# Optimization experiments

Measured on AMD Instinct MI355X. Metric: run time of the kernel, lower is better.

## Reference

```python
import jax, jax.numpy as jnp
import numpy as np

B, S = 128, 32
C = [4, 8, 16, 32]
DN = ('NDHWC', 'DHWIO', 'NDHWC')


def _conv(x, w, stride=1, pad=None):
    k = w.shape[0]
    if pad is None:
        pad = [((k - 1) // 2, k // 2)] * 3  # k=3 -> (1,1); k=4 -> (1,2) as in scn even-kernel convention
    return jax.lax.conv_general_dilated(x, w, (stride,) * 3, pad, dimension_numbers=DN)


def _bn_relu(x, g, b, mask, eps=1e-4):
    # BatchNormLeakyReLU with leakiness=0 (ReLU); stats over ACTIVE voxels only, per channel
    cnt = jnp.maximum(mask.sum(), 1.0)
    mean = (x * mask).sum(axis=(0, 1, 2, 3)) / cnt
    var = (((x - mean) ** 2) * mask).sum(axis=(0, 1, 2, 3)) / cnt
    y = (x - mean) * jax.lax.rsqrt(var + eps) * g + b
    return jnp.maximum(y, 0.0) * mask


def _pool_mask(m):
    # scn.Convolution k=2 s=2: output site active iff any input in its 2^3 receptive field is active
    return jax.lax.reduce_window(m, 0.0, jax.lax.max, (1, 2, 2, 2, 1), (1, 2, 2, 2, 1), 'VALID')


def _up_mask(m):
    # scn.FullConvolution k=2 s=2: each active input activates its full 2^3 output block
    return jnp.repeat(jnp.repeat(jnp.repeat(m, 2, 1), 2, 2), 2, 3)


def _encoder(vox, maskraw, wp, enc, dec, wo):
    mask = (maskraw == 0).astype(vox.dtype)
    x = vox * mask
    x = _conv(x, wp) * mask  # prepare: submanifold conv 1 -> m=4
    for (g, b, ws, wd) in enc:  # 3 non-empty encoding stages (i < num_strides-1)
        x = _bn_relu(x, g, b, mask)
        x = _conv(x, ws) * mask               # submanifold conv k=3
        x = _conv(x, wd, stride=2, pad=[(0, 0)] * 3)  # strided Convolution k=2 s=2
        mask = _pool_mask(mask)
        x = x * mask
    # SparseToDense + view(-1, C*s^3) in NCDHW layout
    hidden = jnp.transpose(x, (0, 4, 1, 2, 3)).reshape(x.shape[0], -1)
    for (g, b, wu, ws3, ws4) in dec:  # i = 2, 1, 0
        x = _bn_relu(x, g, b, mask)
        x = jax.lax.conv_transpose(x, wu, (2, 2, 2), 'VALID', dimension_numbers=DN)  # FullConvolution
        mask = _up_mask(mask)
        x = x * mask
        x = _conv(x, ws3) * mask              # submanifold conv k=3 (end of decoding_conv1)
        mask = mask * (x[..., :1] > 0).astype(x.dtype)  # SparsifyFCS (applied twice; idempotent)
        x = x * mask
        x = _conv(x, ws4) * mask              # submanifold conv k=4 (decoding_conv2)
    out = _conv(x, wo) * mask                 # output: submanifold conv m -> 1
    return hidden, out


def setup_inputs():
    key = jax.random.key(0)
    ks = iter(jax.random.split(key, 64))

    def rnd(shape, s=0.1):
        return jax.random.normal(next(ks), shape, jnp.float32) * s

    inp = {}
    inp['vox'] = jax.random.normal(next(ks), (B, S, S, S, 1), jnp.float32)
    inp['maskraw'] = jax.random.randint(next(ks), (B, S, S, S, 1), 0, 10, jnp.int32)
    inp['wp'] = rnd((3, 3, 3, 1, C[0]))
    for i in range(3):
        ci, co = C[i], C[i + 1]
        inp[f'g_e{i}'] = 1.0 + rnd((ci,))
        inp[f'b_e{i}'] = rnd((ci,))
        inp[f'ws_e{i}'] = rnd((3, 3, 3, ci, ci))
        inp[f'wd_e{i}'] = rnd((2, 2, 2, ci, co))
    for j, i in enumerate([2, 1, 0]):
        ci, co = C[i + 1], C[i]
        inp[f'g_d{j}'] = 1.0 + rnd((ci,))
        inp[f'b_d{j}'] = rnd((ci,))
        inp[f'wu_d{j}'] = rnd((2, 2, 2, ci, co))
        inp[f'ws3_d{j}'] = rnd((3, 3, 3, co, co))
        inp[f'ws4_d{j}'] = rnd((4, 4, 4, co, co))
    inp['wo'] = rnd((3, 3, 3, C[0], 1))
    return inp


def reference(vox, maskraw, wp, g_e0, b_e0, ws_e0, wd_e0, g_e1, b_e1, ws_e1, wd_e1, g_e2, b_e2, ws_e2, wd_e2, g_d0, b_d0, wu_d0, ws3_d0, ws4_d0, g_d1, b_d1, wu_d1, ws3_d1, ws4_d1, g_d2, b_d2, wu_d2, ws3_d2, ws4_d2, wo):
    enc = [(g_e0, b_e0, ws_e0, wd_e0), (g_e1, b_e1, ws_e1, wd_e1), (g_e2, b_e2, ws_e2, wd_e2)]
    dec = [(g_d0, b_d0, wu_d0, ws3_d0, ws4_d0), (g_d1, b_d1, wu_d1, ws3_d1, ws4_d1), (g_d2, b_d2, wu_d2, ws3_d2, ws4_d2)]
    return _encoder(vox, maskraw, wp, enc, dec, wo)
```

## Files before the change

### kernel.cpp

```cpp
#include <hip/hip_runtime.h>

using u8 = unsigned char;

__global__ void mask_init_k(const int* __restrict__ mr, u8* __restrict__ m, int N) {
    int i = blockIdx.x * blockDim.x + threadIdx.x;
    if (i < N) m[i] = (mr[i] == 0) ? 1 : 0;
}

template <int SO>
__global__ void pool_k(const u8* __restrict__ mi, u8* __restrict__ mo) {
    const int N = 128 * SO * SO * SO;
    constexpr int SI = 2 * SO;
    int v = blockIdx.x * blockDim.x + threadIdx.x;
    if (v >= N) return;
    int t = v;
    int x = t % SO; t /= SO;
    int y = t % SO; t /= SO;
    int z = t % SO;
    int n = t / SO;
    u8 m = 0;
    for (int kd = 0; kd < 2; kd++)
        for (int kh = 0; kh < 2; kh++)
            for (int kw = 0; kw < 2; kw++)
                m |= mi[((n * SI + 2 * z + kd) * SI + 2 * y + kh) * SI + 2 * x + kw];
    mo[v] = m;
}


__global__ void prep4t_k(const float* __restrict__ vox, const u8* __restrict__ m,
                         const float* __restrict__ wp, float* __restrict__ out) {
    __shared__ float til[6 * 10 * 35];
    int bid = blockIdx.x;
    int y0 = (bid & 3) << 3, z0 = ((bid >> 2) & 7) << 2, n = bid >> 5;
    for (int t = threadIdx.x; t < 6 * 10 * 35; t += 256) {
        int x_ = t % 35;
        int rr = t / 35;
        int yy = rr % 10, zz = rr / 10;
        int gx = x_ - 1, gy = y0 + yy - 1, gz = z0 + zz - 1;
        float v = 0.f;
        if ((unsigned)gx < 32u && (unsigned)gy < 32u && (unsigned)gz < 32u) {
            int gi = ((n * 32 + gz) * 32 + gy) * 32 + gx;
            if (m[gi]) v = vox[gi];
        }
        til[t] = v;
    }
    __syncthreads();
    int tx = threadIdx.x;
    int xg = tx & 7, ly = (tx >> 3) & 7, lz = tx >> 6;
    int xb = xg << 2;
    int vbase = ((n * 32 + z0 + lz) * 32 + y0 + ly) * 32 + xb;
    u8 om[4];
#pragma unroll
    for (int j = 0; j < 4; j++) om[j] = m[vbase + j];
    float acc[4][4];
#pragma unroll
    for (int j = 0; j < 4; j++)
#pragma unroll
        for (int co = 0; co < 4; co++) acc[j][co] = 0.f;
    for (int kd = 0; kd < 3; kd++) {
        for (int kh = 0; kh < 3; kh++) {
            const float* rowp = &til[((lz + kd) * 10 + ly + kh) * 35 + xb];
            float col[6];
#pragma unroll
            for (int c = 0; c < 6; c++) col[c] = rowp[c];
            const float* wrow = wp + ((kd * 3 + kh) * 3) * 4;
#pragma unroll
            for (int kw = 0; kw < 3; kw++) {
                const float* wt = wrow + kw * 4;
#pragma unroll
                for (int j = 0; j < 4; j++) {
                    float xv = col[j + kw];
#pragma unroll
                    for (int co = 0; co < 4; co++) acc[j][co] += xv * wt[co];
                }
            }
        }
    }
#pragma unroll
    for (int j = 0; j < 4; j++)
#pragma unroll
        for (int co = 0; co < 4; co++)
            out[(size_t)(vbase + j) * 4 + co] = om[j] ? acc[j][co] : 0.f;
}

__global__ void convbn4t_k(const float* __restrict__ in, const float* __restrict__ w,
                           const u8* __restrict__ mask, const double* __restrict__ params,
                           float* __restrict__ out) {
    __shared__ float4 til[6 * 10 * 35];
    float sc[4], sh[4];
#pragma unroll
    for (int c = 0; c < 4; c++) { sc[c] = (float)params[c]; sh[c] = (float)params[4 + c]; }
    int bid = blockIdx.x;
    int y0 = (bid & 3) << 3, z0 = ((bid >> 2) & 7) << 2, n = bid >> 5;
    for (int t = threadIdx.x; t < 6 * 10 * 35; t += 256) {
        int x_ = t % 35;
        int rr = t / 35;
        int yy = rr % 10, zz = rr / 10;
        int gx = x_ - 1, gy = y0 + yy - 1, gz = z0 + zz - 1;
        float4 v = make_float4(0.f, 0.f, 0.f, 0.f);
        if ((unsigned)gx < 32u && (unsigned)gy < 32u && (unsigned)gz < 32u) {
            int gi = ((n * 32 + gz) * 32 + gy) * 32 + gx;
            if (mask[gi]) {
                float4 r = *(const float4*)(in + (size_t)gi * 4);
                v.x = fmaxf(r.x * sc[0] + sh[0], 0.f);
                v.y = fmaxf(r.y * sc[1] + sh[1], 0.f);
                v.z = fmaxf(r.z * sc[2] + sh[2], 0.f);
                v.w = fmaxf(r.w * sc[3] + sh[3], 0.f);
            }
        }
        til[t] = v;
    }
    __syncthreads();
    int tx = threadIdx.x;
    int xg = tx & 7, ly = (tx >> 3) & 7, lz = tx >> 6;
    int xb = xg << 2;
    int vbase = ((n * 32 + z0 + lz) * 32 + y0 + ly) * 32 + xb;
    u8 om[4];
#pragma unroll
    for (int j = 0; j < 4; j++) om[j] = mask[vbase + j];
    float acc[4][4];
#pragma unroll
    for (int j = 0; j < 4; j++)
#pragma unroll
        for (int co = 0; co < 4; co++) acc[j][co] = 0.f;
    for (int kd = 0; kd < 3; kd++) {
        for (int kh = 0; kh < 3; kh++) {
            const float4* rowp = &til[((lz + kd) * 10 + ly + kh) * 35 + xb];
            float col[6][4];
#pragma unroll
            for (int c = 0; c < 6; c++) {
                float4 t4 = rowp[c];
                col[c][0] = t4.x; col[c][1] = t4.y; col[c][2] = t4.z; col[c][3] = t4.w;
            }
            const float* wrow = w + ((kd * 3 + kh) * 3) * 16;
#pragma unroll
            for (int kw = 0; kw < 3; kw++) {
                const float* wt = wrow + kw * 16;
#pragma unroll
                for (int j = 0; j < 4; j++) {
#pragma unroll
                    for (int ci = 0; ci < 4; ci++) {
                        float xv = col[j + kw][ci];
#pragma unroll
                        for (int co = 0; co < 4; co++) acc[j][co] += xv * wt[ci * 4 + co];
                    }
                }
            }
        }
    }
#pragma unroll
    for (int j = 0; j < 4; j++)
#pragma unroll
        for (int co = 0; co < 4; co++)
            out[(size_t)(vbase + j) * 4 + co] = om[j] ? acc[j][co] : 0.f;
}

__global__ void conv3s4t_k(const float* __restrict__ in, const float* __restrict__ w,
                           const u8* __restrict__ pmask, u8* __restrict__ nmask,
                           float* __restrict__ out, double delta) {
    __shared__ float4 til[6 * 10 * 35];
    int bid = blockIdx.x;
    int y0 = (bid & 3) << 3, z0 = ((bid >> 2) & 7) << 2, n = bid >> 5;
    for (int t = threadIdx.x; t < 6 * 10 * 35; t += 256) {
        int x_ = t % 35;
        int rr = t / 35;
        int yy = rr % 10, zz = rr / 10;
        int gx = x_ - 1, gy = y0 + yy - 1, gz = z0 + zz - 1;
        float4 v = make_float4(0.f, 0.f, 0.f, 0.f);
        if ((unsigned)gx < 32u && (unsigned)gy < 32u && (unsigned)gz < 32u)
            v = *(const float4*)(in + (size_t)(((n * 32 + gz) * 32 + gy) * 32 + gx) * 4);
        til[t] = v;
    }
    __syncthreads();
    int tx = threadIdx.x;
    int xg = tx & 7, ly = (tx >> 3) & 7, lz = tx >> 6;
    int xb = xg << 2;
    int gy = y0 + ly, gz = z0 + lz;
    int vbase = ((n * 32 + gz) * 32 + gy) * 32 + xb;
    int pbase = ((n * 16 + (gz >> 1)) * 16 + (gy >> 1)) * 16 + (xb >> 1);
    u8 pm[4];
    pm[0] = pm[1] = pmask[pbase];
    pm[2] = pm[3] = pmask[pbase + 1];
    double acc0[4], asum[4];
    float accf[4][4];
#pragma unroll
    for (int j = 0; j < 4; j++) {
        acc0[j] = 0.0; asum[j] = 0.0;
#pragma unroll
        for (int co = 0; co < 4; co++) accf[j][co] = 0.f;
    }
    for (int kd = 0; kd < 3; kd++) {
        for (int kh = 0; kh < 3; kh++) {
            const float4* rowp = &til[((lz + kd) * 10 + ly + kh) * 35 + xb];
            float col[6][4];
#pragma unroll
            for (int c = 0; c < 6; c++) {
                float4 t4 = rowp[c];
                col[c][0] = t4.x; col[c][1] = t4.y; col[c][2] = t4.z; col[c][3] = t4.w;
            }
            const float* wrow = w + ((kd * 3 + kh) * 3) * 16;
#pragma unroll
            for (int kw = 0; kw < 3; kw++) {
                const float* wt = wrow + kw * 16;
#pragma unroll
                for (int j = 0; j < 4; j++) {
#pragma unroll
                    for (int ci = 0; ci < 4; ci++) {
                        float xv = col[j + kw][ci];
                        double term = (double)xv * (double)wt[ci * 4 + 0];
                        acc0[j] += term;
                        asum[j] += fabs(term);
#pragma unroll
                        for (int co = 1; co < 4; co++) accf[j][co] += xv * wt[ci * 4 + co];
                    }
                }
            }
        }
    }
#pragma unroll
    for (int j = 0; j < 4; j++) {
        u8 nm = (pm[j] && (acc0[j] > -delta * asum[j])) ? 1 : 0;
        nmask[vbase + j] = nm;
        out[(size_t)(vbase + j) * 4 + 0] = nm ? (float)acc0[j] : 0.f;
#pragma unroll
        for (int co = 1; co < 4; co++) out[(size_t)(vbase + j) * 4 + co] = nm ? accf[j][co] : 0.f;
    }
}

__global__ void conv4x4t_k(const float* __restrict__ in, const float* __restrict__ w,
                           const u8* __restrict__ outmask, float* __restrict__ out) {
    __shared__ float4 til[7 * 11 * 35];
    int bid = blockIdx.x;
    int y0 = (bid & 3) << 3, z0 = ((bid >> 2) & 7) << 2, n = bid >> 5;
    for (int t = threadIdx.x; t < 7 * 11 * 35; t += 256) {
        int x_ = t % 35;
        int rr = t / 35;
        int yy = rr % 11, zz = rr / 11;
        int gx = x_ - 1, gy = y0 + yy - 1, gz = z0 + zz - 1;
        float4 v = make_float4(0.f, 0.f, 0.f, 0.f);
        if ((unsigned)gx < 32u && (unsigned)gy < 32u && (unsigned)gz < 32u)
            v = *(const float4*)(in + (size_t)(((n * 32 + gz) * 32 + gy) * 32 + gx) * 4);
        til[t] = v;
    }
    __syncthreads();
    int tx = threadIdx.x;
    int xg = tx & 7, ly = (tx >> 3) & 7, lz = tx >> 6;
    int xb = xg << 2;
    int vbase = ((n * 32 + z0 + lz) * 32 + y0 + ly) * 32 + xb;
    u8 om[4];
#pragma unroll
    for (int j = 0; j < 4; j++) om[j] = outmask[vbase + j];
    float acc[4][4];
#pragma unroll
    for (int j = 0; j < 4; j++)
#pragma unroll
        for (int co = 0; co < 4; co++) acc[j][co] = 0.f;
    for (int kd = 0; kd < 4; kd++) {
        for (int kh = 0; kh < 4; kh++) {
            const float4* rowp = &til[((lz + kd) * 11 + ly + kh) * 35 + xb];
            float col[7][4];
#pragma unroll
            for (int c = 0; c < 7; c++) {
                float4 t4 = rowp[c];
                col[c][0] = t4.x; col[c][1] = t4.y; col[c][2] = t4.z; col[c][3] = t4.w;
            }
            const float* wrow = w + ((kd * 4 + kh) * 4) * 16;
#pragma unroll
            for (int kw = 0; kw < 4; kw++) {
                const float* wt = wrow + kw * 16;
#pragma unroll
                for (int j = 0; j < 4; j++) {
#pragma unroll
                    for (int ci = 0; ci < 4; ci++) {
                        float xv = col[j + kw][ci];
#pragma unroll
                        for (int co = 0; co < 4; co++) acc[j][co] += xv * wt[ci * 4 + co];
                    }
                }
            }
        }
    }
#pragma unroll
    for (int j = 0; j < 4; j++)
#pragma unroll
        for (int co = 0; co < 4; co++)
            out[(size_t)(vbase + j) * 4 + co] = om[j] ? acc[j][co] : 0.f;
}

__global__ void outconv4t_k(const float* __restrict__ in, const float* __restrict__ w,
                            const u8* __restrict__ mask, float* __restrict__ out) {
    __shared__ float4 til[6 * 10 * 35];
    int bid = blockIdx.x;
    int y0 = (bid & 3) << 3, z0 = ((bid >> 2) & 7) << 2, n = bid >> 5;
    for (int t = threadIdx.x; t < 6 * 10 * 35; t += 256) {
        int x_ = t % 35;
        int rr = t / 35;
        int yy = rr % 10, zz = rr / 10;
        int gx = x_ - 1, gy = y0 + yy - 1, gz = z0 + zz - 1;
        float4 v = make_float4(0.f, 0.f, 0.f, 0.f);
        if ((unsigned)gx < 32u && (unsigned)gy < 32u && (unsigned)gz < 32u)
            v = *(const float4*)(in + (size_t)(((n * 32 + gz) * 32 + gy) * 32 + gx) * 4);
        til[t] = v;
    }
    __syncthreads();
    int tx = threadIdx.x;
    int xg = tx & 7, ly = (tx >> 3) & 7, lz = tx >> 6;
    int xb = xg << 2;
    int vbase = ((n * 32 + z0 + lz) * 32 + y0 + ly) * 32 + xb;
    u8 om[4];
#pragma unroll
    for (int j = 0; j < 4; j++) om[j] = mask[vbase + j];
    float acc[4] = {0.f, 0.f, 0.f, 0.f};
    for (int kd = 0; kd < 3; kd++) {
        for (int kh = 0; kh < 3; kh++) {
            const float4* rowp = &til[((lz + kd) * 10 + ly + kh) * 35 + xb];
            float col[6][4];
#pragma unroll
            for (int c = 0; c < 6; c++) {
                float4 t4 = rowp[c];
                col[c][0] = t4.x; col[c][1] = t4.y; col[c][2] = t4.z; col[c][3] = t4.w;
            }
            const float* wrow = w + ((kd * 3 + kh) * 3) * 4;
#pragma unroll
            for (int kw = 0; kw < 3; kw++) {
                const float* wt = wrow + kw * 4;
#pragma unroll
                for (int j = 0; j < 4; j++) {
#pragma unroll
                    for (int ci = 0; ci < 4; ci++) acc[j] += col[j + kw][ci] * wt[ci];
                }
            }
        }
    }
#pragma unroll
    for (int j = 0; j < 4; j++) out[vbase + j] = om[j] ? acc[j] : 0.f;
}


__global__ void convbn8_k(const float* __restrict__ in, const float* __restrict__ w,
                          const u8* __restrict__ mask, const double* __restrict__ params,
                          float* __restrict__ out) {
    __shared__ float4 til[4][330];
    __shared__ float wl[27 * 256];
    float sc[16], sh[16];
#pragma unroll
    for (int c = 0; c < 16; c++) { sc[c] = (float)params[c]; sh[c] = (float)params[16 + c]; }
    int z = blockIdx.x & 7, n = blockIdx.x >> 3;
    for (int t = threadIdx.x; t < 27 * 256; t += 256) wl[t] = w[t];
    for (int t = threadIdx.x; t < 300; t += 256) {
        int xx = t % 10;
        int rr = t / 10;
        int yy = rr % 10, zz = rr / 10;
        int gx = xx - 1, gy = yy - 1, gz = z + zz - 1;
        float v[16];
#pragma unroll
        for (int c = 0; c < 16; c++) v[c] = 0.f;
        if ((unsigned)gx < 8u && (unsigned)gy < 8u && (unsigned)gz < 8u) {
            int gi = ((n * 8 + gz) * 8 + gy) * 8 + gx;
            if (mask[gi]) {
                const float* ip = in + (size_t)gi * 16;
#pragma unroll
                for (int c = 0; c < 16; c++) v[c] = fmaxf(ip[c] * sc[c] + sh[c], 0.f);
            }
        }
        int s = (zz * 10 + yy) * 11 + xx;
#pragma unroll
        for (int q = 0; q < 4; q++)
            til[q][s] = make_float4(v[4 * q], v[4 * q + 1], v[4 * q + 2], v[4 * q + 3]);
    }
    __syncthreads();
    int x = threadIdx.x & 7, y = (threadIdx.x >> 3) & 7, cq = threadIdx.x >> 6;
    int v = ((n * 8 + z) * 8 + y) * 8 + x;
    u8 om = mask[v];
    float acc[4] = {0.f, 0.f, 0.f, 0.f};
    for (int kd = 0; kd < 3; kd++) {
        for (int kh = 0; kh < 3; kh++) {
            int rbase = (kd * 10 + y + kh) * 11 + x;
            const float* wrow = wl + ((kd * 3 + kh) * 3) * 256;
#pragma unroll
            for (int kw = 0; kw < 3; kw++) {
                int s = rbase + kw;
                float4 q0 = til[0][s], q1 = til[1][s], q2 = til[2][s], q3 = til[3][s];
                float xs[16] = {q0.x, q0.y, q0.z, q0.w, q1.x, q1.y, q1.z, q1.w,
                                q2.x, q2.y, q2.z, q2.w, q3.x, q3.y, q3.z, q3.w};
                const float* wt = wrow + kw * 256 + cq * 4;
#pragma unroll
                for (int ci = 0; ci < 16; ci++) {
                    float xv = xs[ci];
                    float4 w4 = *(const float4*)(wt + ci * 16);
                    acc[0] += xv * w4.x; acc[1] += xv * w4.y;
                    acc[2] += xv * w4.z; acc[3] += xv * w4.w;
                }
            }
        }
    }
    float* op = out + (size_t)v * 16 + cq * 4;
#pragma unroll
    for (int j = 0; j < 4; j++) op[j] = om ? acc[j] : 0.f;
}

__global__ void conv3s8_k(const float* __restrict__ in, const float* __restrict__ w,
                          const u8* __restrict__ pmask, u8* __restrict__ nmask,
                          float* __restrict__ out, double delta) {
    __shared__ float4 til[4][330];
    __shared__ float wl[27 * 256];
    __shared__ u8 nmsh[64];
    int z = blockIdx.x & 7, n = blockIdx.x >> 3;
    for (int t = threadIdx.x; t < 27 * 256; t += 256) wl[t] = w[t];
    for (int t = threadIdx.x; t < 300; t += 256) {
        int xx = t % 10;
        int rr = t / 10;
        int yy = rr % 10, zz = rr / 10;
        int gx = xx - 1, gy = yy - 1, gz = z + zz - 1;
        float4 v0 = make_float4(0.f, 0.f, 0.f, 0.f), v1 = v0, v2 = v0, v3 = v0;
        if ((unsigned)gx < 8u && (unsigned)gy < 8u && (unsigned)gz < 8u) {
            const float4* ip = (const float4*)(in + (size_t)(((n * 8 + gz) * 8 + gy) * 8 + gx) * 16);
            v0 = ip[0]; v1 = ip[1]; v2 = ip[2]; v3 = ip[3];
        }
        int s = (zz * 10 + yy) * 11 + xx;
        til[0][s] = v0; til[1][s] = v1; til[2][s] = v2; til[3][s] = v3;
    }
    __syncthreads();
    int x = threadIdx.x & 7, y = (threadIdx.x >> 3) & 7, cq = threadIdx.x >> 6;
    int v = ((n * 8 + z) * 8 + y) * 8 + x;
    double acc0 = 0.0, asum = 0.0;
    float acc[4] = {0.f, 0.f, 0.f, 0.f};
    for (int kd = 0; kd < 3; kd++) {
        for (int kh = 0; kh < 3; kh++) {
            int rbase = (kd * 10 + y + kh) * 11 + x;
            const float* wrow = wl + ((kd * 3 + kh) * 3) * 256;
#pragma unroll
            for (int kw = 0; kw < 3; kw++) {
                int s = rbase + kw;
                float4 q0 = til[0][s], q1 = til[1][s], q2 = til[2][s], q3 = til[3][s];
                float xs[16] = {q0.x, q0.y, q0.z, q0.w, q1.x, q1.y, q1.z, q1.w,
                                q2.x, q2.y, q2.z, q2.w, q3.x, q3.y, q3.z, q3.w};
                const float* wt0 = wrow + kw * 256;
                if (cq == 0) {
#pragma unroll
                    for (int ci = 0; ci < 16; ci++) {
                        float xv = xs[ci];
                        double term = (double)xv * (double)wt0[ci * 16];
                        acc0 += term;
                        asum += fabs(term);
#pragma unroll
                        for (int j = 1; j < 4; j++) acc[j] += xv * wt0[ci * 16 + j];
                    }
                } else {
                    const float* wt = wt0 + cq * 4;
#pragma unroll
                    for (int ci = 0; ci < 16; ci++) {
                        float xv = xs[ci];
                        float4 w4 = *(const float4*)(wt + ci * 16);
                        acc[0] += xv * w4.x; acc[1] += xv * w4.y;
                        acc[2] += xv * w4.z; acc[3] += xv * w4.w;
                    }
                }
            }
        }
    }
    if (cq == 0) {
        u8 pm = pmask[((n * 4 + (z >> 1)) * 4 + (y >> 1)) * 4 + (x >> 1)];
        u8 nm = (pm && (acc0 > -delta * asum)) ? 1 : 0;
        nmsh[y * 8 + x] = nm;
        nmask[v] = nm;
    }
    __syncthreads();
    u8 nm = nmsh[y * 8 + x];
    float* op = out + (size_t)v * 16 + cq * 4;
    if (cq == 0) {
        op[0] = nm ? (float)acc0 : 0.f;
#pragma unroll
        for (int j = 1; j < 4; j++) op[j] = nm ? acc[j] : 0.f;
    } else {
#pragma unroll
        for (int j = 0; j < 4; j++) op[j] = nm ? acc[j] : 0.f;
    }
}

__global__ void conv48_k(const float* __restrict__ in, const float* __restrict__ w,
                         const u8* __restrict__ outmask, float* __restrict__ out) {
    __shared__ float4 til[4][572];
    __shared__ float wl[16 * 256];
    int z = blockIdx.x & 7, n = blockIdx.x >> 3;
    for (int t = threadIdx.x; t < 484; t += 256) {
        int xx = t % 11;
        int rr = t / 11;
        int yy = rr % 11, zz = rr / 11;
        int gx = xx - 1, gy = yy - 1, gz = z + zz - 1;
        float4 v0 = make_float4(0.f, 0.f, 0.f, 0.f), v1 = v0, v2 = v0, v3 = v0;
        if ((unsigned)gx < 8u && (unsigned)gy < 8u && (unsigned)gz < 8u) {
            const float4* ip = (const float4*)(in + (size_t)(((n * 8 + gz) * 8 + gy) * 8 + gx) * 16);
            v0 = ip[0]; v1 = ip[1]; v2 = ip[2]; v3 = ip[3];
        }
        int s = (zz * 11 + yy) * 13 + xx;
        til[0][s] = v0; til[1][s] = v1; til[2][s] = v2; til[3][s] = v3;
    }
    int x = threadIdx.x & 7, y = (threadIdx.x >> 3) & 7, cq = threadIdx.x >> 6;
    int v = ((n * 8 + z) * 8 + y) * 8 + x;
    u8 om = outmask[v];
    float acc[4] = {0.f, 0.f, 0.f, 0.f};
    for (int kd = 0; kd < 4; kd++) {
        __syncthreads();
        for (int t = threadIdx.x; t < 16 * 256; t += 256) wl[t] = w[kd * 16 * 256 + t];
        __syncthreads();
        for (int kh = 0; kh < 4; kh++) {
            int rbase = (kd * 11 + y + kh) * 13 + x;
            const float* wrow = wl + (kh * 4) * 256;
#pragma unroll
            for (int kw = 0; kw < 4; kw++) {
                int s = rbase + kw;
                float4 q0 = til[0][s], q1 = til[1][s], q2 = til[2][s], q3 = til[3][s];
                float xs[16] = {q0.x, q0.y, q0.z, q0.w, q1.x, q1.y, q1.z, q1.w,
                                q2.x, q2.y, q2.z, q2.w, q3.x, q3.y, q3.z, q3.w};
                const float* wt = wrow + kw * 256 + cq * 4;
#pragma unroll
                for (int ci = 0; ci < 16; ci++) {
                    float xv = xs[ci];
                    float4 w4 = *(const float4*)(wt + ci * 16);
                    acc[0] += xv * w4.x; acc[1] += xv * w4.y;
                    acc[2] += xv * w4.z; acc[3] += xv * w4.w;
                }
            }
        }
    }
    float* op = out + (size_t)v * 16 + cq * 4;
#pragma unroll
    for (int j = 0; j < 4; j++) op[j] = om ? acc[j] : 0.f;
}


template <int K, int CIN, int COUT, int S>
__global__ void conv_k(const float* __restrict__ in, const float* __restrict__ w,
                       const u8* __restrict__ outmask, float* __restrict__ out) {
    __shared__ float wl[K * K * K * CIN * COUT];
    for (int t = threadIdx.x; t < K * K * K * CIN * COUT; t += 256) wl[t] = w[t];
    __syncthreads();
    const int N = 128 * S * S * S;
    int v = blockIdx.x * blockDim.x + threadIdx.x;
    if (v >= N) return;
    if (!outmask[v]) {
#pragma unroll
        for (int co = 0; co < COUT; co++) out[(size_t)v * COUT + co] = 0.f;
        return;
    }
    int t = v;
    int x = t % S; t /= S;
    int y = t % S; t /= S;
    int z = t % S;
    int n = t / S;
    float acc[COUT];
#pragma unroll
    for (int co = 0; co < COUT; co++) acc[co] = 0.f;
    constexpr int PLO = (K - 1) / 2;
    for (int kd = 0; kd < K; kd++) {
        int zz = z + kd - PLO; if ((unsigned)zz >= (unsigned)S) continue;
        for (int kh = 0; kh < K; kh++) {
            int yy = y + kh - PLO; if ((unsigned)yy >= (unsigned)S) continue;
            for (int kw = 0; kw < K; kw++) {
                int xx = x + kw - PLO; if ((unsigned)xx >= (unsigned)S) continue;
                int sv = ((n * S + zz) * S + yy) * S + xx;
                const float* ip = in + (size_t)sv * CIN;
                const float* wpk = wl + ((kd * K + kh) * K + kw) * CIN * COUT;
#pragma unroll
                for (int ci = 0; ci < CIN; ci++) {
                    float xv = ip[ci];
#pragma unroll
                    for (int co = 0; co < COUT; co++) acc[co] += xv * wpk[ci * COUT + co];
                }
            }
        }
    }
#pragma unroll
    for (int co = 0; co < COUT; co++) out[(size_t)v * COUT + co] = acc[co];
}

template <int CIN, int COUT, int S>
__global__ void convbn_k(const float* __restrict__ in, const float* __restrict__ w,
                         const u8* __restrict__ mask, const double* __restrict__ params,
                         float* __restrict__ out) {
    __shared__ float wl[27 * CIN * COUT];
    for (int t = threadIdx.x; t < 27 * CIN * COUT; t += 256) wl[t] = w[t];
    __syncthreads();
    const int N = 128 * S * S * S;
    int v = blockIdx.x * blockDim.x + threadIdx.x;
    if (v >= N) return;
    if (!mask[v]) {
#pragma unroll
        for (int co = 0; co < COUT; co++) out[(size_t)v * COUT + co] = 0.f;
        return;
    }
    int t = v;
    int x = t % S; t /= S;
    int y = t % S; t /= S;
    int z = t % S;
    int n = t / S;
    float sc[CIN], sh[CIN];
#pragma unroll
    for (int c = 0; c < CIN; c++) { sc[c] = (float)params[c]; sh[c] = (float)params[CIN + c]; }
    float acc[COUT];
#pragma unroll
    for (int co = 0; co < COUT; co++) acc[co] = 0.f;
    for (int kd = 0; kd < 3; kd++) {
        int zz = z + kd - 1; if ((unsigned)zz >= (unsigned)S) continue;
        for (int kh = 0; kh < 3; kh++) {
            int yy = y + kh - 1; if ((unsigned)yy >= (unsigned)S) continue;
            for (int kw = 0; kw < 3; kw++) {
                int xx = x + kw - 1; if ((unsigned)xx >= (unsigned)S) continue;
                int sv = ((n * S + zz) * S + yy) * S + xx;
                if (!mask[sv]) continue;
                const float* ip = in + (size_t)sv * CIN;
                const float* wpk = wl + ((kd * 3 + kh) * 3 + kw) * CIN * COUT;
#pragma unroll
                for (int ci = 0; ci < CIN; ci++) {
                    float yv = fmaxf(ip[ci] * sc[ci] + sh[ci], 0.f);
#pragma unroll
                    for (int co = 0; co < COUT; co++) acc[co] += yv * wpk[ci * COUT + co];
                }
            }
        }
    }
#pragma unroll
    for (int co = 0; co < COUT; co++) out[(size_t)v * COUT + co] = acc[co];
}

template <int CIN, int COUT, int S>
__global__ void conv3s_k(const float* __restrict__ in, const float* __restrict__ w,
                         const u8* __restrict__ pmask, u8* __restrict__ nmask,
                         float* __restrict__ out, double delta) {
    __shared__ float wl[27 * CIN * COUT];
    for (int t = threadIdx.x; t < 27 * CIN * COUT; t += 256) wl[t] = w[t];
    __syncthreads();
    const int N = 128 * S * S * S;
    constexpr int SP = S / 2;
    int v = blockIdx.x * blockDim.x + threadIdx.x;
    if (v >= N) return;
    int t = v;
    int x = t % S; t /= S;
    int y = t % S; t /= S;
    int z = t % S;
    int n = t / S;
    int pidx = ((n * SP + (z >> 1)) * SP + (y >> 1)) * SP + (x >> 1);
    if (!pmask[pidx]) {
        nmask[v] = 0;
#pragma unroll
        for (int co = 0; co < COUT; co++) out[(size_t)v * COUT + co] = 0.f;
        return;
    }
    double acc0 = 0.0, asum = 0.0;
    float acc[COUT];
#pragma unroll
    for (int co = 0; co < COUT; co++) acc[co] = 0.f;
    for (int kd = 0; kd < 3; kd++) {
        int zz = z + kd - 1; if ((unsigned)zz >= (unsigned)S) continue;
        for (int kh = 0; kh < 3; kh++) {
            int yy = y + kh - 1; if ((unsigned)yy >= (unsigned)S) continue;
            for (int kw = 0; kw < 3; kw++) {
                int xx = x + kw - 1; if ((unsigned)xx >= (unsigned)S) continue;
                int sv = ((n * S + zz) * S + yy) * S + xx;
                const float* ip = in + (size_t)sv * CIN;
                const float* wpk = wl + ((kd * 3 + kh) * 3 + kw) * CIN * COUT;
#pragma unroll
                for (int ci = 0; ci < CIN; ci++) {
                    float xv = ip[ci];
                    double term = (double)xv * (double)wpk[ci * COUT + 0];
                    acc0 += term;
                    asum += fabs(term);
#pragma unroll
                    for (int co = 1; co < COUT; co++) acc[co] += xv * wpk[ci * COUT + co];
                }
            }
        }
    }
    u8 nm = (acc0 > -delta * asum) ? 1 : 0;
    nmask[v] = nm;
    out[(size_t)v * COUT + 0] = nm ? (float)acc0 : 0.f;
#pragma unroll
    for (int co = 1; co < COUT; co++) out[(size_t)v * COUT + co] = nm ? acc[co] : 0.f;
}

template <int CIN, int COUT, int SO>
__global__ void down_k(const float* __restrict__ in, const float* __restrict__ w,
                       const u8* __restrict__ outmask, float* __restrict__ out) {
    const int N = 128 * SO * SO * SO;
    constexpr int SI = 2 * SO;
    int v = blockIdx.x * blockDim.x + threadIdx.x;
    if (v >= N) return;
    if (!outmask[v]) {
#pragma unroll
        for (int co = 0; co < COUT; co++) out[(size_t)v * COUT + co] = 0.f;
        return;
    }
    int t = v;
    int x = t % SO; t /= SO;
    int y = t % SO; t /= SO;
    int z = t % SO;
    int n = t / SO;
    float acc[COUT];
#pragma unroll
    for (int co = 0; co < COUT; co++) acc[co] = 0.f;
    for (int kd = 0; kd < 2; kd++)
        for (int kh = 0; kh < 2; kh++)
            for (int kw = 0; kw < 2; kw++) {
                int sv = ((n * SI + 2 * z + kd) * SI + 2 * y + kh) * SI + 2 * x + kw;
                const float* ip = in + (size_t)sv * CIN;
                const float* wpk = w + ((kd * 2 + kh) * 2 + kw) * CIN * COUT;
#pragma unroll
                for (int ci = 0; ci < CIN; ci++) {
                    float xv = ip[ci];
#pragma unroll
                    for (int co = 0; co < COUT; co++) acc[co] += xv * wpk[ci * COUT + co];
                }
            }
#pragma unroll
    for (int co = 0; co < COUT; co++) out[(size_t)v * COUT + co] = acc[co];
}

template <int CIN, int COUT, int SI>
__global__ void upbn_k(const float* __restrict__ in, const float* __restrict__ w,
                       const u8* __restrict__ inmask, const double* __restrict__ params,
                       float* __restrict__ out) {
    constexpr int SO = 2 * SI;
    const int N = 128 * SO * SO * SO;
    int v = blockIdx.x * blockDim.x + threadIdx.x;
    if (v >= N) return;
    int t = v;
    int x = t % SO; t /= SO;
    int y = t % SO; t /= SO;
    int z = t % SO;
    int n = t / SO;
    int sv = ((n * SI + (z >> 1)) * SI + (y >> 1)) * SI + (x >> 1);
    if (!inmask[sv]) {
#pragma unroll
        for (int co = 0; co < COUT; co++) out[(size_t)v * COUT + co] = 0.f;
        return;
    }
    int tap = ((1 - (z & 1)) * 2 + (1 - (y & 1))) * 2 + (1 - (x & 1));
    const float* wpk = w + tap * CIN * COUT;
    const float* ip = in + (size_t)sv * CIN;
    float acc[COUT];
#pragma unroll
    for (int co = 0; co < COUT; co++) acc[co] = 0.f;
#pragma unroll
    for (int ci = 0; ci < CIN; ci++) {
        float yv = fmaxf(ip[ci] * (float)params[ci] + (float)params[CIN + ci], 0.f);
#pragma unroll
        for (int co = 0; co < COUT; co++) acc[co] += yv * wpk[ci * COUT + co];
    }
#pragma unroll
    for (int co = 0; co < COUT; co++) out[(size_t)v * COUT + co] = acc[co];
}

template <int C>
__global__ void bn_reduce_k(const float* __restrict__ x, const u8* __restrict__ m, int N,
                            double* __restrict__ partial) {
    double cnt = 0.0, sx[C], s2[C];
#pragma unroll
    for (int c = 0; c < C; c++) { sx[c] = 0.0; s2[c] = 0.0; }
    int stride = gridDim.x * blockDim.x;
    for (int v = blockIdx.x * blockDim.x + threadIdx.x; v < N; v += stride) {
        if (!m[v]) continue;
        cnt += 1.0;
#pragma unroll
        for (int c = 0; c < C; c++) {
            double xv = (double)x[(size_t)v * C + c];
            sx[c] += xv;
            s2[c] += xv * xv;
        }
    }
#pragma unroll
    for (int off = 32; off > 0; off >>= 1) {
        cnt += __shfl_down(cnt, off, 64);
#pragma unroll
        for (int c = 0; c < C; c++) {
            sx[c] += __shfl_down(sx[c], off, 64);
            s2[c] += __shfl_down(s2[c], off, 64);
        }
    }
    __shared__ double sbuf[4][2 * C + 1];
    int wave = threadIdx.x >> 6;
    if ((threadIdx.x & 63) == 0) {
        sbuf[wave][0] = cnt;
#pragma unroll
        for (int c = 0; c < C; c++) {
            sbuf[wave][1 + c] = sx[c];
            sbuf[wave][1 + C + c] = s2[c];
        }
    }
    __syncthreads();
    if (threadIdx.x == 0) {
        double* p = partial + (size_t)blockIdx.x * (2 * C + 1);
        double tcnt = 0.0;
        for (int wv = 0; wv < 4; wv++) tcnt += sbuf[wv][0];
        p[0] = tcnt;
#pragma unroll
        for (int c = 0; c < C; c++) {
            double a = 0.0, b = 0.0;
            for (int wv = 0; wv < 4; wv++) { a += sbuf[wv][1 + c]; b += sbuf[wv][1 + C + c]; }
            p[1 + c] = a;
            p[1 + C + c] = b;
        }
    }
}

template <int C>
__global__ void bn_final_k(const double* __restrict__ partial, int nblocks,
                           const float* __restrict__ g, const float* __restrict__ b,
                           double* __restrict__ params) {
    int c = threadIdx.x;
    if (c >= C) return;
    double cnt = 0.0, sx = 0.0, s2 = 0.0;
    for (int bk = 0; bk < nblocks; bk++) {
        const double* p = partial + (size_t)bk * (2 * C + 1);
        cnt += p[0];
        sx += p[1 + c];
        s2 += p[1 + C + c];
    }
    if (cnt < 1.0) cnt = 1.0;
    double mean = sx / cnt;
    double var = s2 / cnt - mean * mean;
    double sc = (double)g[c] / sqrt(var + 1e-4);
    params[c] = sc;
    params[C + c] = (double)b[c] - mean * sc;
}

__global__ void hidden_k(const float* __restrict__ x, float* __restrict__ out) {
    int i = blockIdx.x * blockDim.x + threadIdx.x;
    if (i >= 128 * 2048) return;
    int b = i >> 11;
    int r = i & 2047;
    int c = r >> 6;
    int s = r & 63;
    int d = s >> 4;
    int h = (s >> 2) & 3;
    int w = s & 3;
    out[i] = x[((((b * 4 + d) * 4 + h) * 4 + w) << 5) + c];
}

extern "C" void kernel_launch(void* const* d_in, const int* in_sizes, int n_in,
                              void* d_out, int out_size, void* d_ws, size_t ws_size,
                              hipStream_t stream) {
    const float* vox = (const float*)d_in[0];
    const int* mraw = (const int*)d_in[1];
    const float* wp = (const float*)d_in[2];
    const float* g_e0 = (const float*)d_in[3];
    const float* b_e0 = (const float*)d_in[4];
    const float* ws_e0 = (const float*)d_in[5];
    const float* wd_e0 = (const float*)d_in[6];
    const float* g_e1 = (const float*)d_in[7];
    const float* b_e1 = (const float*)d_in[8];
    const float* ws_e1 = (const float*)d_in[9];
    const float* wd_e1 = (const float*)d_in[10];
    const float* g_e2 = (const float*)d_in[11];
    const float* b_e2 = (const float*)d_in[12];
    const float* ws_e2 = (const float*)d_in[13];
    const float* wd_e2 = (const float*)d_in[14];
    const float* g_d0 = (const float*)d_in[15];
    const float* b_d0 = (const float*)d_in[16];
    const float* wu_d0 = (const float*)d_in[17];
    const float* ws3_d0 = (const float*)d_in[18];
    const float* ws4_d0 = (const float*)d_in[19];
    const float* g_d1 = (const float*)d_in[20];
    const float* b_d1 = (const float*)d_in[21];
    const float* wu_d1 = (const float*)d_in[22];
    const float* ws3_d1 = (const float*)d_in[23];
    const float* ws4_d1 = (const float*)d_in[24];
    const float* g_d2 = (const float*)d_in[25];
    const float* b_d2 = (const float*)d_in[26];
    const float* wu_d2 = (const float*)d_in[27];
    const float* ws3_d2 = (const float*)d_in[28];
    const float* ws4_d2 = (const float*)d_in[29];
    const float* wo = (const float*)d_in[30];
    float* out = (float*)d_out;

    float* wsf = (float*)d_ws;
    size_t offf = 0;
    auto allocf = [&](size_t n) { float* p = wsf + offf; offf += n; return p; };
    float* R1 = allocf(16777216);
    float* R2 = allocf(16777216);
    float* S1 = allocf(1048576);
    float* S2 = allocf(1048576);
    float* T = allocf(262144);
    double* wsd = (double*)(wsf + offf);
    double* partial = wsd;
    double* params = wsd + 16640;
    u8* wsm = (u8*)(wsd + 16640 + 128);
    size_t offm = 0;
    auto allocm = [&](size_t n) { u8* p = wsm + offm; offm += n; return p; };
    u8* m32 = allocm(4194304);
    u8* m16 = allocm(524288);
    u8* m8 = allocm(65536);
    u8* m4 = allocm(8192);
    u8* mD8 = allocm(65536);
    u8* mD16 = allocm(524288);
    u8* mD32 = allocm(4194304);

    const int N32 = 128 * 32768;
    const int N16 = 128 * 4096;
    const int N8 = 128 * 512;
    const int N4 = 128 * 64;
    auto gs = [](int n) { return dim3((n + 255) / 256); };
    auto rbn = [](int n) { int bl = (n + 255) / 256; return bl > 256 ? 256 : bl; };
    dim3 blk(256);
    dim3 tgrid(4096);
    dim3 grid8(1024);

    mask_init_k<<<gs(N32), blk, 0, stream>>>(mraw, m32, N32);
    pool_k<16><<<gs(N16), blk, 0, stream>>>(m32, m16);
    pool_k<8><<<gs(N8), blk, 0, stream>>>(m16, m8);
    pool_k<4><<<gs(N4), blk, 0, stream>>>(m8, m4);

    prep4t_k<<<tgrid, blk, 0, stream>>>(vox, m32, wp, R1);
    int nb0 = rbn(N32);
    bn_reduce_k<4><<<dim3(nb0), blk, 0, stream>>>(R1, m32, N32, partial);
    bn_final_k<4><<<1, 64, 0, stream>>>(partial, nb0, g_e0, b_e0, params);
    convbn4t_k<<<tgrid, blk, 0, stream>>>(R1, ws_e0, m32, params, R2);
    down_k<4, 8, 16><<<gs(N16), blk, 0, stream>>>(R2, wd_e0, m16, R1);

    int nb1 = rbn(N16);
    bn_reduce_k<8><<<dim3(nb1), blk, 0, stream>>>(R1, m16, N16, partial);
    bn_final_k<8><<<1, 64, 0, stream>>>(partial, nb1, g_e1, b_e1, params);
    convbn_k<8, 8, 16><<<gs(N16), blk, 0, stream>>>(R1, ws_e1, m16, params, R2);
    down_k<8, 16, 8><<<gs(N8), blk, 0, stream>>>(R2, wd_e1, m8, S1);

    int nb2 = rbn(N8);
    bn_reduce_k<16><<<dim3(nb2), blk, 0, stream>>>(S1, m8, N8, partial);
    bn_final_k<16><<<1, 64, 0, stream>>>(partial, nb2, g_e2, b_e2, params);
    convbn8_k<<<grid8, blk, 0, stream>>>(S1, ws_e2, m8, params, S2);
    down_k<16, 32, 4><<<gs(N4), blk, 0, stream>>>(S2, wd_e2, m4, T);

    hidden_k<<<gs(128 * 2048), blk, 0, stream>>>(T, out);

    int nb3 = rbn(N4);
    bn_reduce_k<32><<<dim3(nb3), blk, 0, stream>>>(T, m4, N4, partial);
    bn_final_k<32><<<1, 64, 0, stream>>>(partial, nb3, g_d0, b_d0, params);
    upbn_k<32, 16, 4><<<gs(N8), blk, 0, stream>>>(T, wu_d0, m4, params, S1);
    conv3s8_k<<<grid8, blk, 0, stream>>>(S1, ws3_d0, m4, mD8, S2, 4e-7);
    conv48_k<<<grid8, blk, 0, stream>>>(S2, ws4_d0, mD8, S1);

    int nb4 = rbn(N8);
    bn_reduce_k<16><<<dim3(nb4), blk, 0, stream>>>(S1, mD8, N8, partial);
    bn_final_k<16><<<1, 64, 0, stream>>>(partial, nb4, g_d1, b_d1, params);
    upbn_k<16, 8, 8><<<gs(N16), blk, 0, stream>>>(S1, wu_d1, mD8, params, R1);
    conv3s_k<8, 8, 16><<<gs(N16), blk, 0, stream>>>(R1, ws3_d1, mD8, mD16, R2, 4e-7);
    conv_k<4, 8, 8, 16><<<gs(N16), blk, 0, stream>>>(R2, ws4_d1, mD16, R1);

    int nb5 = rbn(N16);
    bn_reduce_k<8><<<dim3(nb5), blk, 0, stream>>>(R1, mD16, N16, partial);
    bn_final_k<8><<<1, 64, 0, stream>>>(partial, nb5, g_d2, b_d2, params);
    upbn_k<8, 4, 16><<<gs(N32), blk, 0, stream>>>(R1, wu_d2, mD16, params, R2);
    conv3s4t_k<<<tgrid, blk, 0, stream>>>(R2, ws3_d2, mD16, mD32, R1, 0.0);
    conv4x4t_k<<<tgrid, blk, 0, stream>>>(R1, ws4_d2, mD32, R2);
    outconv4t_k<<<tgrid, blk, 0, stream>>>(R2, wo, mD32, out + 262144);
}
```

Before: 1.480 ms.

## Add shared-memory tiled convs for 16^3 stage and drop unused asum in 32^3 sparsify

Three per-voxel 16^3 convolution kernels (encoder conv+BN, decoder sparsify conv, decoder k=4 conv) are replaced with tiled versions. Each block stages an input halo tile and the weights in LDS, and each thread computes two voxels along x. This removes redundant global gathers, mask-driven divergence and per-voxel early exits. Separately, the 32^3 sparsify kernel was always called with delta=0, so it now drops the double-precision abs-sum accumulator and tests acc0>0 directly. The tiled kernels compute every voxel, including inactive ones, so they give up the work skipped at roughly 10% occupancy in exchange for regular, coalesced access.

```diff
diff --git a/kernel.cpp b/kernel.cpp
--- a/kernel.cpp
+++ b/kernel.cpp
@@ -157,7 +157,7 @@
 
 __global__ void conv3s4t_k(const float* __restrict__ in, const float* __restrict__ w,
                            const u8* __restrict__ pmask, u8* __restrict__ nmask,
-                           float* __restrict__ out, double delta) {
+                           float* __restrict__ out) {
     __shared__ float4 til[6 * 10 * 35];
     int bid = blockIdx.x;
     int y0 = (bid & 3) << 3, z0 = ((bid >> 2) & 7) << 2, n = bid >> 5;
@@ -181,11 +181,11 @@
     u8 pm[4];
     pm[0] = pm[1] = pmask[pbase];
     pm[2] = pm[3] = pmask[pbase + 1];
-    double acc0[4], asum[4];
+    double acc0[4];
     float accf[4][4];
 #pragma unroll
     for (int j = 0; j < 4; j++) {
-        acc0[j] = 0.0; asum[j] = 0.0;
+        acc0[j] = 0.0;
 #pragma unroll
         for (int co = 0; co < 4; co++) accf[j][co] = 0.f;
     }
@@ -207,9 +207,7 @@
 #pragma unroll
                     for (int ci = 0; ci < 4; ci++) {
                         float xv = col[j + kw][ci];
-                        double term = (double)xv * (double)wt[ci * 4 + 0];
-                        acc0[j] += term;
-                        asum[j] += fabs(term);
+                        acc0[j] += (double)xv * (double)wt[ci * 4 + 0];
 #pragma unroll
                         for (int co = 1; co < 4; co++) accf[j][co] += xv * wt[ci * 4 + co];
                     }
@@ -219,7 +217,7 @@
     }
 #pragma unroll
     for (int j = 0; j < 4; j++) {
-        u8 nm = (pm[j] && (acc0[j] > -delta * asum[j])) ? 1 : 0;
+        u8 nm = (pm[j] && (acc0[j] > 0.0)) ? 1 : 0;
         nmask[vbase + j] = nm;
         out[(size_t)(vbase + j) * 4 + 0] = nm ? (float)acc0[j] : 0.f;
 #pragma unroll
@@ -334,6 +332,218 @@
     }
 #pragma unroll
     for (int j = 0; j < 4; j++) out[vbase + j] = om[j] ? acc[j] : 0.f;
+}
+
+
+__global__ void convbn16t_k(const float* __restrict__ in, const float* __restrict__ w,
+                            const u8* __restrict__ mask, const double* __restrict__ params,
+                            float* __restrict__ out) {
+    __shared__ float4 til[2][1140];
+    __shared__ float wl[1728];
+    float sc[8], sh[8];
+#pragma unroll
+    for (int c = 0; c < 8; c++) { sc[c] = (float)params[c]; sh[c] = (float)params[8 + c]; }
+    int bid = blockIdx.x;
+    int y0 = (bid & 1) << 3, z0 = ((bid >> 1) & 3) << 2, n = bid >> 3;
+    for (int t = threadIdx.x; t < 1728; t += 256) wl[t] = w[t];
+    for (int t = threadIdx.x; t < 1140; t += 256) {
+        int x_ = t % 19;
+        int rr = t / 19;
+        int yy = rr % 10, zz = rr / 10;
+        int gx = x_ - 1, gy = y0 + yy - 1, gz = z0 + zz - 1;
+        float v[8];
+#pragma unroll
+        for (int c = 0; c < 8; c++) v[c] = 0.f;
+        if ((unsigned)gx < 16u && (unsigned)gy < 16u && (unsigned)gz < 16u) {
+            int gi = ((n * 16 + gz) * 16 + gy) * 16 + gx;
+            if (mask[gi]) {
+                const float* ip = in + (size_t)gi * 8;
+#pragma unroll
+                for (int c = 0; c < 8; c++) v[c] = fmaxf(ip[c] * sc[c] + sh[c], 0.f);
+            }
+        }
+        til[0][t] = make_float4(v[0], v[1], v[2], v[3]);
+        til[1][t] = make_float4(v[4], v[5], v[6], v[7]);
+    }
+    __syncthreads();
+    int xg = threadIdx.x & 7, ly = (threadIdx.x >> 3) & 7, lz = threadIdx.x >> 6;
+    int xb = xg << 1;
+    int vbase = ((n * 16 + z0 + lz) * 16 + y0 + ly) * 16 + xb;
+    u8 om[2] = {mask[vbase], mask[vbase + 1]};
+    float acc[2][8];
+#pragma unroll
+    for (int j = 0; j < 2; j++)
+#pragma unroll
+        for (int co = 0; co < 8; co++) acc[j][co] = 0.f;
+    for (int kd = 0; kd < 3; kd++) {
+        for (int kh = 0; kh < 3; kh++) {
+            int rbase = ((lz + kd) * 10 + ly + kh) * 19 + xb;
+            float col[4][8];
+#pragma unroll
+            for (int c = 0; c < 4; c++) {
+                float4 a = til[0][rbase + c], b = til[1][rbase + c];
+                col[c][0] = a.x; col[c][1] = a.y; col[c][2] = a.z; col[c][3] = a.w;
+                col[c][4] = b.x; col[c][5] = b.y; col[c][6] = b.z; col[c][7] = b.w;
+            }
+            const float* wrow = wl + ((kd * 3 + kh) * 3) * 64;
+#pragma unroll
+            for (int kw = 0; kw < 3; kw++) {
+                const float* wt = wrow + kw * 64;
+#pragma unroll
+                for (int j = 0; j < 2; j++) {
+#pragma unroll
+                    for (int ci = 0; ci < 8; ci++) {
+                        float xv = col[j + kw][ci];
+#pragma unroll
+                        for (int co = 0; co < 8; co++) acc[j][co] += xv * wt[ci * 8 + co];
+                    }
+                }
+            }
+        }
+    }
+#pragma unroll
+    for (int j = 0; j < 2; j++)
+#pragma unroll
+        for (int co = 0; co < 8; co++)
+            out[(size_t)(vbase + j) * 8 + co] = om[j] ? acc[j][co] : 0.f;
+}
+
+__global__ void conv3s16t_k(const float* __restrict__ in, const float* __restrict__ w,
+                            const u8* __restrict__ pmask, u8* __restrict__ nmask,
+                            float* __restrict__ out, double delta) {
+    __shared__ float4 til[2][1140];
+    __shared__ float wl[1728];
+    int bid = blockIdx.x;
+    int y0 = (bid & 1) << 3, z0 = ((bid >> 1) & 3) << 2, n = bid >> 3;
+    for (int t = threadIdx.x; t < 1728; t += 256) wl[t] = w[t];
+    for (int t = threadIdx.x; t < 1140; t += 256) {
+        int x_ = t % 19;
+        int rr = t / 19;
+        int yy = rr % 10, zz = rr / 10;
+        int gx = x_ - 1, gy = y0 + yy - 1, gz = z0 + zz - 1;
+        float4 a = make_float4(0.f, 0.f, 0.f, 0.f), b = a;
+        if ((unsigned)gx < 16u && (unsigned)gy < 16u && (unsigned)gz < 16u) {
+            const float4* ip = (const float4*)(in + (size_t)(((n * 16 + gz) * 16 + gy) * 16 + gx) * 8);
+            a = ip[0]; b = ip[1];
+        }
+        til[0][t] = a;
+        til[1][t] = b;
+    }
+    __syncthreads();
+    int xg = threadIdx.x & 7, ly = (threadIdx.x >> 3) & 7, lz = threadIdx.x >> 6;
+    int xb = xg << 1;
+    int gy = y0 + ly, gz = z0 + lz;
+    int vbase = ((n * 16 + gz) * 16 + gy) * 16 + xb;
+    u8 pm = pmask[((n * 8 + (gz >> 1)) * 8 + (gy >> 1)) * 8 + (xb >> 1)];
+    double acc0[2], asum[2];
+    float accf[2][8];
+#pragma unroll
+    for (int j = 0; j < 2; j++) {
+        acc0[j] = 0.0; asum[j] = 0.0;
+#pragma unroll
+        for (int co = 0; co < 8; co++) accf[j][co] = 0.f;
+    }
+    for (int kd = 0; kd < 3; kd++) {
+        for (int kh = 0; kh < 3; kh++) {
+            int rbase = ((lz + kd) * 10 + ly + kh) * 19 + xb;
+            float col[4][8];
+#pragma unroll
+            for (int c = 0; c < 4; c++) {
+                float4 a = til[0][rbase + c], b = til[1][rbase + c];
+                col[c][0] = a.x; col[c][1] = a.y; col[c][2] = a.z; col[c][3] = a.w;
+                col[c][4] = b.x; col[c][5] = b.y; col[c][6] = b.z; col[c][7] = b.w;
+            }
+            const float* wrow = wl + ((kd * 3 + kh) * 3) * 64;
+#pragma unroll
+            for (int kw = 0; kw < 3; kw++) {
+                const float* wt = wrow + kw * 64;
+#pragma unroll
+                for (int j = 0; j < 2; j++) {
+#pragma unroll
+                    for (int ci = 0; ci < 8; ci++) {
+                        float xv = col[j + kw][ci];
+                        double term = (double)xv * (double)wt[ci * 8 + 0];
+                        acc0[j] += term;
+                        asum[j] += fabs(term);
+#pragma unroll
+                        for (int co = 1; co < 8; co++) accf[j][co] += xv * wt[ci * 8 + co];
+                    }
+                }
+            }
+        }
+    }
+#pragma unroll
+    for (int j = 0; j < 2; j++) {
+        u8 nm = (pm && (acc0[j] > -delta * asum[j])) ? 1 : 0;
+        nmask[vbase + j] = nm;
+        out[(size_t)(vbase + j) * 8 + 0] = nm ? (float)acc0[j] : 0.f;
+#pragma unroll
+        for (int co = 1; co < 8; co++) out[(size_t)(vbase + j) * 8 + co] = nm ? accf[j][co] : 0.f;
+    }
+}
+
+__global__ void conv416t_k(const float* __restrict__ in, const float* __restrict__ w,
+                           const u8* __restrict__ outmask, float* __restrict__ out) {
+    __shared__ float4 til[2][1463];
+    __shared__ float wl[1024];
+    int bid = blockIdx.x;
+    int y0 = (bid & 1) << 3, z0 = ((bid >> 1) & 3) << 2, n = bid >> 3;
+    for (int t = threadIdx.x; t < 1463; t += 256) {
+        int x_ = t % 19;
+        int rr = t / 19;
+        int yy = rr % 11, zz = rr / 11;
+        int gx = x_ - 1, gy = y0 + yy - 1, gz = z0 + zz - 1;
+        float4 a = make_float4(0.f, 0.f, 0.f, 0.f), b = a;
+        if ((unsigned)gx < 16u && (unsigned)gy < 16u && (unsigned)gz < 16u) {
+            const float4* ip = (const float4*)(in + (size_t)(((n * 16 + gz) * 16 + gy) * 16 + gx) * 8);
+            a = ip[0]; b = ip[1];
+        }
+        til[0][t] = a;
+        til[1][t] = b;
+    }
+    int xg = threadIdx.x & 7, ly = (threadIdx.x >> 3) & 7, lz = threadIdx.x >> 6;
+    int xb = xg << 1;
+    int vbase = ((n * 16 + z0 + lz) * 16 + y0 + ly) * 16 + xb;
+    u8 om[2] = {outmask[vbase], outmask[vbase + 1]};
+    float acc[2][8];
+#pragma unroll
+    for (int j = 0; j < 2; j++)
+#pragma unroll
+        for (int co = 0; co < 8; co++) acc[j][co] = 0.f;
+    for (int kd = 0; kd < 4; kd++) {
+        __syncthreads();
+        for (int t = threadIdx.x; t < 1024; t += 256) wl[t] = w[kd * 1024 + t];
+        __syncthreads();
+        for (int kh = 0; kh < 4; kh++) {
+            int rbase = ((lz + kd) * 11 + ly + kh) * 19 + xb;
+            float col[5][8];
+#pragma unroll
+            for (int c = 0; c < 5; c++) {
+                float4 a = til[0][rbase + c], b = til[1][rbase + c];
+                col[c][0] = a.x; col[c][1] = a.y; col[c][2] = a.z; col[c][3] = a.w;
+                col[c][4] = b.x; col[c][5] = b.y; col[c][6] = b.z; col[c][7] = b.w;
+            }
+            const float* wrow = wl + (kh * 4) * 64;
+#pragma unroll
+            for (int kw = 0; kw < 4; kw++) {
+                const float* wt = wrow + kw * 64;
+#pragma unroll
+                for (int j = 0; j < 2; j++) {
+#pragma unroll
+                    for (int ci = 0; ci < 8; ci++) {
+                        float xv = col[j + kw][ci];
+#pragma unroll
+                        for (int co = 0; co < 8; co++) acc[j][co] += xv * wt[ci * 8 + co];
+                    }
+                }
+            }
+        }
+    }
+#pragma unroll
+    for (int j = 0; j < 2; j++)
+#pragma unroll
+        for (int co = 0; co < 8; co++)
+            out[(size_t)(vbase + j) * 8 + co] = om[j] ? acc[j][co] : 0.f;
 }
 
 
@@ -529,155 +739,6 @@
     for (int j = 0; j < 4; j++) op[j] = om ? acc[j] : 0.f;
 }
 
-
-template <int K, int CIN, int COUT, int S>
-__global__ void conv_k(const float* __restrict__ in, const float* __restrict__ w,
-                       const u8* __restrict__ outmask, float* __restrict__ out) {
-    __shared__ float wl[K * K * K * CIN * COUT];
-    for (int t = threadIdx.x; t < K * K * K * CIN * COUT; t += 256) wl[t] = w[t];
-    __syncthreads();
-    const int N = 128 * S * S * S;
-    int v = blockIdx.x * blockDim.x + threadIdx.x;
-    if (v >= N) return;
-    if (!outmask[v]) {
-#pragma unroll
-        for (int co = 0; co < COUT; co++) out[(size_t)v * COUT + co] = 0.f;
-        return;
-    }
-    int t = v;
-    int x = t % S; t /= S;
-    int y = t % S; t /= S;
-    int z = t % S;
-    int n = t / S;
-    float acc[COUT];
-#pragma unroll
-    for (int co = 0; co < COUT; co++) acc[co] = 0.f;
-    constexpr int PLO = (K - 1) / 2;
-    for (int kd = 0; kd < K; kd++) {
-        int zz = z + kd - PLO; if ((unsigned)zz >= (unsigned)S) continue;
-        for (int kh = 0; kh < K; kh++) {
-            int yy = y + kh - PLO; if ((unsigned)yy >= (unsigned)S) continue;
-            for (int kw = 0; kw < K; kw++) {
-                int xx = x + kw - PLO; if ((unsigned)xx >= (unsigned)S) continue;
-                int sv = ((n * S + zz) * S + yy) * S + xx;
-                const float* ip = in + (size_t)sv * CIN;
-                const float* wpk = wl + ((kd * K + kh) * K + kw) * CIN * COUT;
-#pragma unroll
-                for (int ci = 0; ci < CIN; ci++) {
-                    float xv = ip[ci];
-#pragma unroll
-                    for (int co = 0; co < COUT; co++) acc[co] += xv * wpk[ci * COUT + co];
-                }
-            }
-        }
-    }
-#pragma unroll
-    for (int co = 0; co < COUT; co++) out[(size_t)v * COUT + co] = acc[co];
-}
-
-template <int CIN, int COUT, int S>
-__global__ void convbn_k(const float* __restrict__ in, const float* __restrict__ w,
-                         const u8* __restrict__ mask, const double* __restrict__ params,
-                         float* __restrict__ out) {
-    __shared__ float wl[27 * CIN * COUT];
-    for (int t = threadIdx.x; t < 27 * CIN * COUT; t += 256) wl[t] = w[t];
-    __syncthreads();
-    const int N = 128 * S * S * S;
-    int v = blockIdx.x * blockDim.x + threadIdx.x;
-    if (v >= N) return;
-    if (!mask[v]) {
-#pragma unroll
-        for (int co = 0; co < COUT; co++) out[(size_t)v * COUT + co] = 0.f;
-        return;
-    }
-    int t = v;
-    int x = t % S; t /= S;
-    int y = t % S; t /= S;
-    int z = t % S;
-    int n = t / S;
-    float sc[CIN], sh[CIN];
-#pragma unroll
-    for (int c = 0; c < CIN; c++) { sc[c] = (float)params[c]; sh[c] = (float)params[CIN + c]; }
-    float acc[COUT];
-#pragma unroll
-    for (int co = 0; co < COUT; co++) acc[co] = 0.f;
-    for (int kd = 0; kd < 3; kd++) {
-        int zz = z + kd - 1; if ((unsigned)zz >= (unsigned)S) continue;
-        for (int kh = 0; kh < 3; kh++) {
-            int yy = y + kh - 1; if ((unsigned)yy >= (unsigned)S) continue;
-            for (int kw = 0; kw < 3; kw++) {
-                int xx = x + kw - 1; if ((unsigned)xx >= (unsigned)S) continue;
-                int sv = ((n * S + zz) * S + yy) * S + xx;
-                if (!mask[sv]) continue;
-                const float* ip = in + (size_t)sv * CIN;
-                const float* wpk = wl + ((kd * 3 + kh) * 3 + kw) * CIN * COUT;
-#pragma unroll
-                for (int ci = 0; ci < CIN; ci++) {
-                    float yv = fmaxf(ip[ci] * sc[ci] + sh[ci], 0.f);
-#pragma unroll
-                    for (int co = 0; co < COUT; co++) acc[co] += yv * wpk[ci * COUT + co];
-                }
-            }
-        }
-    }
-#pragma unroll
-    for (int co = 0; co < COUT; co++) out[(size_t)v * COUT + co] = acc[co];
-}
-
-template <int CIN, int COUT, int S>
-__global__ void conv3s_k(const float* __restrict__ in, const float* __restrict__ w,
-                         const u8* __restrict__ pmask, u8* __restrict__ nmask,
-                         float* __restrict__ out, double delta) {
-    __shared__ float wl[27 * CIN * COUT];
-    for (int t = threadIdx.x; t < 27 * CIN * COUT; t += 256) wl[t] = w[t];
-    __syncthreads();
-    const int N = 128 * S * S * S;
-    constexpr int SP = S / 2;
-    int v = blockIdx.x * blockDim.x + threadIdx.x;
-    if (v >= N) return;
-    int t = v;
-    int x = t % S; t /= S;
-    int y = t % S; t /= S;
-    int z = t % S;
-    int n = t / S;
-    int pidx = ((n * SP + (z >> 1)) * SP + (y >> 1)) * SP + (x >> 1);
-    if (!pmask[pidx]) {
-        nmask[v] = 0;
-#pragma unroll
-        for (int co = 0; co < COUT; co++) out[(size_t)v * COUT + co] = 0.f;
-        return;
-    }
-    double acc0 = 0.0, asum = 0.0;
-    float acc[COUT];
-#pragma unroll
-    for (int co = 0; co < COUT; co++) acc[co] = 0.f;
-    for (int kd = 0; kd < 3; kd++) {
-        int zz = z + kd - 1; if ((unsigned)zz >= (unsigned)S) continue;
-        for (int kh = 0; kh < 3; kh++) {
-            int yy = y + kh - 1; if ((unsigned)yy >= (unsigned)S) continue;
-            for (int kw = 0; kw < 3; kw++) {
-                int xx = x + kw - 1; if ((unsigned)xx >= (unsigned)S) continue;
-                int sv = ((n * S + zz) * S + yy) * S + xx;
-                const float* ip = in + (size_t)sv * CIN;
-                const float* wpk = wl + ((kd * 3 + kh) * 3 + kw) * CIN * COUT;
-#pragma unroll
-                for (int ci = 0; ci < CIN; ci++) {
-                    float xv = ip[ci];
-                    double term = (double)xv * (double)wpk[ci * COUT + 0];
-                    acc0 += term;
-                    asum += fabs(term);
-#pragma unroll
-                    for (int co = 1; co < COUT; co++) acc[co] += xv * wpk[ci * COUT + co];
-                }
-            }
-        }
-    }
-    u8 nm = (acc0 > -delta * asum) ? 1 : 0;
-    nmask[v] = nm;
-    out[(size_t)v * COUT + 0] = nm ? (float)acc0 : 0.f;
-#pragma unroll
-    for (int co = 1; co < COUT; co++) out[(size_t)v * COUT + co] = nm ? acc[co] : 0.f;
-}
 
 template <int CIN, int COUT, int SO>
 __global__ void down_k(const float* __restrict__ in, const float* __restrict__ w,
@@ -903,6 +964,7 @@
     auto rbn = [](int n) { int bl = (n + 255) / 256; return bl > 256 ? 256 : bl; };
     dim3 blk(256);
     dim3 tgrid(4096);
+    dim3 grid16(1024);
     dim3 grid8(1024);
 
     mask_init_k<<<gs(N32), blk, 0, stream>>>(mraw, m32, N32);
@@ -920,7 +982,7 @@
     int nb1 = rbn(N16);
     bn_reduce_k<8><<<dim3(nb1), blk, 0, stream>>>(R1, m16, N16, partial);
     bn_final_k<8><<<1, 64, 0, stream>>>(partial, nb1, g_e1, b_e1, params);
-    convbn_k<8, 8, 16><<<gs(N16), blk, 0, stream>>>(R1, ws_e1, m16, params, R2);
+    convbn16t_k<<<grid16, blk, 0, stream>>>(R1, ws_e1, m16, params, R2);
     down_k<8, 16, 8><<<gs(N8), blk, 0, stream>>>(R2, wd_e1, m8, S1);
 
     int nb2 = rbn(N8);
@@ -942,14 +1004,14 @@
     bn_reduce_k<16><<<dim3(nb4), blk, 0, stream>>>(S1, mD8, N8, partial);
     bn_final_k<16><<<1, 64, 0, stream>>>(partial, nb4, g_d1, b_d1, params);
     upbn_k<16, 8, 8><<<gs(N16), blk, 0, stream>>>(S1, wu_d1, mD8, params, R1);
-    conv3s_k<8, 8, 16><<<gs(N16), blk, 0, stream>>>(R1, ws3_d1, mD8, mD16, R2, 4e-7);
-    conv_k<4, 8, 8, 16><<<gs(N16), blk, 0, stream>>>(R2, ws4_d1, mD16, R1);
+    conv3s16t_k<<<grid16, blk, 0, stream>>>(R1, ws3_d1, mD8, mD16, R2, 4e-7);
+    conv416t_k<<<grid16, blk, 0, stream>>>(R2, ws4_d1, mD16, R1);
 
     int nb5 = rbn(N16);
     bn_reduce_k<8><<<dim3(nb5), blk, 0, stream>>>(R1, mD16, N16, partial);
     bn_final_k<8><<<1, 64, 0, stream>>>(partial, nb5, g_d2, b_d2, params);
     upbn_k<8, 4, 16><<<gs(N32), blk, 0, stream>>>(R1, wu_d2, mD16, params, R2);
-    conv3s4t_k<<<tgrid, blk, 0, stream>>>(R2, ws3_d2, mD16, mD32, R1, 0.0);
+    conv3s4t_k<<<tgrid, blk, 0, stream>>>(R2, ws3_d2, mD16, mD32, R1);
     conv4x4t_k<<<tgrid, blk, 0, stream>>>(R1, ws4_d2, mD32, R2);
     outconv4t_k<<<tgrid, blk, 0, stream>>>(R2, wo, mD32, out + 262144);
 }
```

After: 1.348 ms. 8.9% less time.
